# Performance work log

Measured on AMD Instinct MI355X. Metric: run time of the kernel, lower is better.

## Reference

```python
import jax, jax.numpy as jnp
import numpy as np

N_NODES = 100000
N_EDGES = 1600000
N_FEAT = 64
HIDDEN = 16


def setup_inputs() -> dict:
    key = jax.random.key(0)
    ks = jax.random.split(key, 10)
    x = jax.random.normal(ks[0], (N_NODES, N_FEAT), dtype=jnp.float32)
    edge_index = jax.random.randint(ks[1], (2, N_EDGES), 0, N_NODES, dtype=jnp.int64)
    As = jax.random.normal(ks[2], (2, N_EDGES), dtype=jnp.float32)
    ws_weights = jax.random.normal(ks[3], (2,), dtype=jnp.float32)
    Wl1 = jax.random.normal(ks[4], (N_FEAT, HIDDEN), dtype=jnp.float32) / np.sqrt(N_FEAT)
    bl1 = jnp.zeros((HIDDEN,), dtype=jnp.float32)
    Wr1 = jax.random.normal(ks[5], (N_FEAT, HIDDEN), dtype=jnp.float32) / np.sqrt(N_FEAT)
    Wl2 = jax.random.normal(ks[6], (HIDDEN, 1), dtype=jnp.float32) / np.sqrt(HIDDEN)
    bl2 = jnp.zeros((1,), dtype=jnp.float32)
    Wr2 = jax.random.normal(ks[7], (HIDDEN, 1), dtype=jnp.float32) / np.sqrt(HIDDEN)
    return {"x": x, "edge_index": edge_index, "As": As, "ws_weights": ws_weights,
            "Wl1": Wl1, "bl1": bl1, "Wr1": Wr1, "Wl2": Wl2, "bl2": bl2, "Wr2": Wr2}


def reference(x, edge_index, As, ws_weights, Wl1, bl1, Wr1, Wl2, bl2, Wr2):
    # WeightedSumLayer: weighted sum of per-edge weight vectors
    ewm = jnp.einsum('m,me->e', ws_weights, As)  # [E]
    # edge mask (nonzero weighted sum keeps the edge); instead of slicing to a
    # data-dependent edge count, zero out masked messages (same aggregation).
    mask = (ewm != 0).astype(x.dtype)  # [E]
    src, dst = edge_index[0], edge_index[1]
    n = x.shape[0]

    # SAGEConv layer 1 (aggr='sum'): out = lin_l(sum_j x_j) + lin_r(x)
    msg1 = x[src] * mask[:, None]                             # [E, F]
    agg1 = jax.ops.segment_sum(msg1, dst, num_segments=n)     # [N, F]
    h = jax.nn.relu(agg1 @ Wl1 + bl1 + x @ Wr1)               # [N, H]

    # SAGEConv layer 2
    msg2 = h[src] * mask[:, None]                             # [E, H]
    agg2 = jax.ops.segment_sum(msg2, dst, num_segments=n)     # [N, H]
    out = agg2 @ Wl2 + bl2 + h @ Wr2                          # [N, 1]
    return out
```

## Files before the change

### kernel.cpp

```cpp
#include <hip/hip_runtime.h>
#include <hip/hip_bf16.h>

constexpr int NN = 100000;
constexpr int NE = 1600000;
constexpr int NF = 64;
constexpr int NH = 16;

constexpr int NPB  = 128;
constexpr int LB   = 7;
constexpr int NBKT = (NN + NPB - 1) / NPB;
constexpr int CAP  = 2560;
constexpr int CHUNK = 8192;
constexpr int TB_B  = 512;
constexpr int NBLK_B = (NE + CHUNK - 1) / CHUNK;

__device__ __forceinline__ float bf16_to_f32(unsigned short u) {
    return __uint_as_float(((unsigned int)u) << 16);
}
__device__ __forceinline__ unsigned short f32_to_bf16(float f) {
    __hip_bfloat16 hb = __float2bfloat16(f);
    return *reinterpret_cast<unsigned short*>(&hb);
}

__global__ __launch_bounds__(256)
void k1_node_lin(const float* __restrict__ x,
                 const float* __restrict__ Wl1,
                 const float* __restrict__ Wr1,
                 unsigned short* __restrict__ p,
                 float* __restrict__ r)
{
    __shared__ float sW[2 * NF * NH];
    for (int i = threadIdx.x; i < NF * NH; i += 256) {
        sW[i]           = Wl1[i];
        sW[NF * NH + i] = Wr1[i];
    }
    __syncthreads();

    int n = blockIdx.x * 256 + threadIdx.x;
    if (n >= NN) return;

    float aL[NH], aR[NH];
#pragma unroll
    for (int j = 0; j < NH; ++j) { aL[j] = 0.f; aR[j] = 0.f; }

    const float4* xr = reinterpret_cast<const float4*>(x + (size_t)n * NF);
#pragma unroll
    for (int k4 = 0; k4 < NF / 4; ++k4) {
        float4 v = xr[k4];
        float xs[4] = {v.x, v.y, v.z, v.w};
#pragma unroll
        for (int t = 0; t < 4; ++t) {
            const float* wl = &sW[(k4 * 4 + t) * NH];
            const float* wr = &sW[NF * NH + (k4 * 4 + t) * NH];
#pragma unroll
            for (int j = 0; j < NH; ++j) {
                aL[j] = fmaf(xs[t], wl[j], aL[j]);
                aR[j] = fmaf(xs[t], wr[j], aR[j]);
            }
        }
    }

    unsigned int pu[8];
#pragma unroll
    for (int j2 = 0; j2 < 8; ++j2)
        pu[j2] = (unsigned int)f32_to_bf16(aL[2*j2]) |
                 ((unsigned int)f32_to_bf16(aL[2*j2+1]) << 16);
    uint4* pp = reinterpret_cast<uint4*>(p + (size_t)n * NH);
    pp[0] = make_uint4(pu[0], pu[1], pu[2], pu[3]);
    pp[1] = make_uint4(pu[4], pu[5], pu[6], pu[7]);

    float4* rp = reinterpret_cast<float4*>(r + (size_t)n * NH);
#pragma unroll
    for (int j4 = 0; j4 < NH / 4; ++j4)
        rp[j4] = make_float4(aR[j4*4], aR[j4*4+1], aR[j4*4+2], aR[j4*4+3]);
}

__global__ __launch_bounds__(TB_B)
void k_bucket(const int* __restrict__ ei, const float* __restrict__ As,
              const float* __restrict__ ws,
              int* __restrict__ bcnt, unsigned int* __restrict__ bmem)
{
    __shared__ unsigned int sw[CHUNK];
    __shared__ unsigned int srk[CHUNK];
    __shared__ int lcnt[NBKT];
    __shared__ int lbase[NBKT];
    int tid = threadIdx.x;
    for (int i = tid; i < NBKT; i += TB_B) lcnt[i] = 0;
    __syncthreads();

    int base = blockIdx.x * CHUNK;
    float w0 = ws[0], w1 = ws[1];

#pragma unroll
    for (int j = 0; j < CHUNK / TB_B; ++j) {
        int idx = j * TB_B + tid;
        int e = base + idx;
        unsigned int w = 0, rk = 0xFFFFFFFFu;
        if (e < NE) {
            float ewm = w0 * As[e] + w1 * As[NE + e];
            if (ewm != 0.f) {
                int dst = ei[NE + e];
                int bk  = dst >> LB;
                w  = ((unsigned)ei[e] << LB) | (unsigned)(dst & (NPB - 1));
                int rank = atomicAdd(&lcnt[bk], 1);
                rk = ((unsigned)bk << 13) | (unsigned)rank;
            }
        }
        sw[idx]  = w;
        srk[idx] = rk;
    }
    __syncthreads();

    for (int i = tid; i < NBKT; i += TB_B) {
        int c = lcnt[i];
        lbase[i] = c ? atomicAdd(&bcnt[i], c) : 0;
    }
    __syncthreads();

#pragma unroll
    for (int j = 0; j < CHUNK / TB_B; ++j) {
        int idx = j * TB_B + tid;
        unsigned int rk = srk[idx];
        if (rk != 0xFFFFFFFFu) {
            int bk   = rk >> 13;
            int rank = rk & 0x1FFF;
            int slot = lbase[bk] + rank;
            if (slot < CAP)
                bmem[(size_t)bk * CAP + slot] = sw[idx];
        }
    }
}

__global__ __launch_bounds__(256)
void k_agg1(const int* __restrict__ bcnt, unsigned int* __restrict__ bmem,
            const unsigned short* __restrict__ p, const float* __restrict__ r,
            const float* __restrict__ bl1, const float* __restrict__ Wl2,
            const float* __restrict__ bl2, const float* __restrict__ Wr2,
            float* __restrict__ q, float* __restrict__ out,
            int* __restrict__ gsoff)
{
    __shared__ unsigned int sbm[CAP];
    __shared__ unsigned int ssorted[CAP];
    __shared__ int hist[NPB];
    __shared__ int scan[NPB];
    __shared__ int soff[NPB + 1];

    int b = blockIdx.x;
    int tid = threadIdx.x;
    if (tid < NPB) hist[tid] = 0;
    __syncthreads();

    int cnt = min(bcnt[b], CAP);

    int rk[CAP / 256];
#pragma unroll
    for (int j = 0; j < CAP / 256; ++j) {
        int i = j * 256 + tid;
        if (i < cnt) {
            unsigned int w = bmem[(size_t)b * CAP + i];
            sbm[i] = w;
            rk[j] = atomicAdd(&hist[w & (NPB - 1)], 1);
        }
    }
    __syncthreads();

    if (tid < NPB) scan[tid] = hist[tid];
    __syncthreads();
    for (int off = 1; off < NPB; off <<= 1) {
        int u = (tid < NPB && tid >= off) ? scan[tid - off] : 0;
        __syncthreads();
        if (tid < NPB) scan[tid] += u;
        __syncthreads();
    }
    if (tid < NPB) soff[tid + 1] = scan[tid];
    if (tid == 0) soff[0] = 0;
    __syncthreads();

#pragma unroll
    for (int j = 0; j < CAP / 256; ++j) {
        int i = j * 256 + tid;
        if (i < cnt) {
            unsigned int w = sbm[i];
            ssorted[soff[w & (NPB - 1)] + rk[j]] = w;
        }
    }
    __syncthreads();

    for (int i = tid; i < cnt; i += 256)
        bmem[(size_t)b * CAP + i] = ssorted[i];
    if (tid < NPB + 1)
        gsoff[(size_t)b * (NPB + 1) + tid] = soff[tid];

    int g = tid >> 4, k = tid & 15;
    int n0 = b * NPB;
#pragma unroll
    for (int jj = 0; jj < 8; ++jj) {
        int nl = g * 8 + jj;
        int s = soff[nl], e = soff[nl + 1];
        float a = 0.f;
        int i = s;
        for (; i + 3 < e; i += 4) {
            unsigned w0 = ssorted[i], w1 = ssorted[i+1], w2 = ssorted[i+2], w3 = ssorted[i+3];
            float v0 = bf16_to_f32(p[(size_t)(w0 >> LB) * NH + k]);
            float v1 = bf16_to_f32(p[(size_t)(w1 >> LB) * NH + k]);
            float v2 = bf16_to_f32(p[(size_t)(w2 >> LB) * NH + k]);
            float v3 = bf16_to_f32(p[(size_t)(w3 >> LB) * NH + k]);
            a += (v0 + v1) + (v2 + v3);
        }
        for (; i < e; ++i)
            a += bf16_to_f32(p[(size_t)(ssorted[i] >> LB) * NH + k]);

        int n = n0 + nl;
        if (n < NN) {
            float h = a + r[(size_t)n * NH + k] + bl1[k];
            h = h > 0.f ? h : 0.f;
            float qv = h * Wl2[k];
            float sv = h * Wr2[k];
#pragma unroll
            for (int m = 8; m >= 1; m >>= 1) {
                qv += __shfl_xor(qv, m);
                sv += __shfl_xor(sv, m);
            }
            if (k == 0) {
                q[n]   = qv;
                out[n] = sv + bl2[0];
            }
        }
    }
}

__global__ __launch_bounds__(256)
void k_agg2(const int* __restrict__ gsoff, const unsigned int* __restrict__ bmem,
            const float* __restrict__ q, float* __restrict__ out)
{
    int n = blockIdx.x * 256 + threadIdx.x;
    if (n >= NN) return;
    int b  = n >> LB;
    int dl = n & (NPB - 1);
    int s = gsoff[(size_t)b * (NPB + 1) + dl];
    int e = gsoff[(size_t)b * (NPB + 1) + dl + 1];
    const unsigned int* bm = bmem + (size_t)b * CAP;

    float a = 0.f;
    int i = s;
    for (; i + 3 < e; i += 4) {
        unsigned w0 = bm[i], w1 = bm[i+1], w2 = bm[i+2], w3 = bm[i+3];
        a += (q[w0 >> LB] + q[w1 >> LB]) + (q[w2 >> LB] + q[w3 >> LB]);
    }
    for (; i < e; ++i)
        a += q[bm[i] >> LB];
    out[n] += a;
}

extern "C" void kernel_launch(void* const* d_in, const int* in_sizes, int n_in,
                              void* d_out, int out_size, void* d_ws, size_t ws_size,
                              hipStream_t stream)
{
    const float* x   = (const float*)d_in[0];
    const int*   ei  = (const int*)  d_in[1];
    const float* As  = (const float*)d_in[2];
    const float* ws  = (const float*)d_in[3];
    const float* Wl1 = (const float*)d_in[4];
    const float* bl1 = (const float*)d_in[5];
    const float* Wr1 = (const float*)d_in[6];
    const float* Wl2 = (const float*)d_in[7];
    const float* bl2 = (const float*)d_in[8];
    const float* Wr2 = (const float*)d_in[9];
    float* out = (float*)d_out;

    unsigned short* p     = (unsigned short*)d_ws;
    float*          r     = (float*)(p + (size_t)NN * NH);
    float*          q     = r + (size_t)NN * NH;
    int*            bcnt  = (int*)(q + NN);
    int*            gsoff = bcnt + NBKT;
    unsigned int*   bmem  = (unsigned int*)(gsoff + (size_t)NBKT * (NPB + 1));

    hipMemsetAsync(bcnt, 0, NBKT * sizeof(int), stream);

    k1_node_lin<<<(NN + 255) / 256, 256, 0, stream>>>(x, Wl1, Wr1, p, r);
    k_bucket<<<NBLK_B, TB_B, 0, stream>>>(ei, As, ws, bcnt, bmem);
    k_agg1<<<NBKT, 256, 0, stream>>>(bcnt, bmem, p, r, bl1, Wl2, bl2, Wr2, q, out, gsoff);
    k_agg2<<<(NN + 255) / 256, 256, 0, stream>>>(gsoff, bmem, q, out);
}
```

Baseline: 181.0 us.

## Fuse node-linear and edge-bucketing kernels into one interleaved-role launch

```diff
diff --git a/kernel.cpp b/kernel.cpp
--- a/kernel.cpp
+++ b/kernel.cpp
@@ -10,9 +10,12 @@
 constexpr int LB   = 7;
 constexpr int NBKT = (NN + NPB - 1) / NPB;
 constexpr int CAP  = 2560;
-constexpr int CHUNK = 8192;
-constexpr int TB_B  = 512;
-constexpr int NBLK_B = (NE + CHUNK - 1) / CHUNK;
+constexpr int CHUNK = 4096;
+constexpr int NBLK_B  = (NE + CHUNK - 1) / CHUNK;
+constexpr int NBLK_K1 = (NN + 255) / 256;
+
+constexpr int SMEM_BYTES = (CHUNK * 2 + 2 * NBKT * 4) > (2 * NF * NH * 4)
+                         ? (CHUNK * 2 + 2 * NBKT * 4) : (2 * NF * NH * 4);
 
 __device__ __forceinline__ float bf16_to_f32(unsigned short u) {
     return __uint_as_float(((unsigned int)u) << 16);
@@ -23,110 +26,109 @@
 }
 
 __global__ __launch_bounds__(256)
-void k1_node_lin(const float* __restrict__ x,
-                 const float* __restrict__ Wl1,
-                 const float* __restrict__ Wr1,
-                 unsigned short* __restrict__ p,
-                 float* __restrict__ r)
-{
-    __shared__ float sW[2 * NF * NH];
-    for (int i = threadIdx.x; i < NF * NH; i += 256) {
-        sW[i]           = Wl1[i];
-        sW[NF * NH + i] = Wr1[i];
-    }
-    __syncthreads();
-
-    int n = blockIdx.x * 256 + threadIdx.x;
-    if (n >= NN) return;
-
-    float aL[NH], aR[NH];
-#pragma unroll
-    for (int j = 0; j < NH; ++j) { aL[j] = 0.f; aR[j] = 0.f; }
-
-    const float4* xr = reinterpret_cast<const float4*>(x + (size_t)n * NF);
-#pragma unroll
-    for (int k4 = 0; k4 < NF / 4; ++k4) {
-        float4 v = xr[k4];
-        float xs[4] = {v.x, v.y, v.z, v.w};
-#pragma unroll
-        for (int t = 0; t < 4; ++t) {
-            const float* wl = &sW[(k4 * 4 + t) * NH];
-            const float* wr = &sW[NF * NH + (k4 * 4 + t) * NH];
-#pragma unroll
-            for (int j = 0; j < NH; ++j) {
-                aL[j] = fmaf(xs[t], wl[j], aL[j]);
-                aR[j] = fmaf(xs[t], wr[j], aR[j]);
-            }
-        }
-    }
-
-    unsigned int pu[8];
-#pragma unroll
-    for (int j2 = 0; j2 < 8; ++j2)
-        pu[j2] = (unsigned int)f32_to_bf16(aL[2*j2]) |
-                 ((unsigned int)f32_to_bf16(aL[2*j2+1]) << 16);
-    uint4* pp = reinterpret_cast<uint4*>(p + (size_t)n * NH);
-    pp[0] = make_uint4(pu[0], pu[1], pu[2], pu[3]);
-    pp[1] = make_uint4(pu[4], pu[5], pu[6], pu[7]);
-
-    float4* rp = reinterpret_cast<float4*>(r + (size_t)n * NH);
-#pragma unroll
-    for (int j4 = 0; j4 < NH / 4; ++j4)
-        rp[j4] = make_float4(aR[j4*4], aR[j4*4+1], aR[j4*4+2], aR[j4*4+3]);
-}
-
-__global__ __launch_bounds__(TB_B)
-void k_bucket(const int* __restrict__ ei, const float* __restrict__ As,
-              const float* __restrict__ ws,
-              int* __restrict__ bcnt, unsigned int* __restrict__ bmem)
-{
-    __shared__ unsigned int sw[CHUNK];
-    __shared__ unsigned int srk[CHUNK];
-    __shared__ int lcnt[NBKT];
-    __shared__ int lbase[NBKT];
-    int tid = threadIdx.x;
-    for (int i = tid; i < NBKT; i += TB_B) lcnt[i] = 0;
-    __syncthreads();
-
-    int base = blockIdx.x * CHUNK;
-    float w0 = ws[0], w1 = ws[1];
-
-#pragma unroll
-    for (int j = 0; j < CHUNK / TB_B; ++j) {
-        int idx = j * TB_B + tid;
-        int e = base + idx;
-        unsigned int w = 0, rk = 0xFFFFFFFFu;
-        if (e < NE) {
-            float ewm = w0 * As[e] + w1 * As[NE + e];
-            if (ewm != 0.f) {
+void k_fused(const float* __restrict__ x,
+             const float* __restrict__ Wl1,
+             const float* __restrict__ Wr1,
+             unsigned short* __restrict__ p,
+             float* __restrict__ r,
+             const int* __restrict__ ei, const float* __restrict__ As,
+             const float* __restrict__ ws,
+             int* __restrict__ bcnt, unsigned int* __restrict__ bmem)
+{
+    __shared__ __align__(16) char smem[SMEM_BYTES];
+    int role = blockIdx.x & 1;
+    int rb   = blockIdx.x >> 1;
+    int tid  = threadIdx.x;
+
+    if (role == 0) {
+        float* sW = (float*)smem;
+        for (int i = tid; i < NF * NH; i += 256) {
+            sW[i]           = Wl1[i];
+            sW[NF * NH + i] = Wr1[i];
+        }
+        __syncthreads();
+
+        int n = rb * 256 + tid;
+        if (n >= NN) return;
+
+        float aL[NH], aR[NH];
+#pragma unroll
+        for (int j = 0; j < NH; ++j) { aL[j] = 0.f; aR[j] = 0.f; }
+
+        const float4* xr = reinterpret_cast<const float4*>(x + (size_t)n * NF);
+#pragma unroll
+        for (int k4 = 0; k4 < NF / 4; ++k4) {
+            float4 v = xr[k4];
+            float xs[4] = {v.x, v.y, v.z, v.w};
+#pragma unroll
+            for (int t = 0; t < 4; ++t) {
+                const float* wl = &sW[(k4 * 4 + t) * NH];
+                const float* wr = &sW[NF * NH + (k4 * 4 + t) * NH];
+#pragma unroll
+                for (int j = 0; j < NH; ++j) {
+                    aL[j] = fmaf(xs[t], wl[j], aL[j]);
+                    aR[j] = fmaf(xs[t], wr[j], aR[j]);
+                }
+            }
+        }
+
+        unsigned int pu[8];
+#pragma unroll
+        for (int j2 = 0; j2 < 8; ++j2)
+            pu[j2] = (unsigned int)f32_to_bf16(aL[2*j2]) |
+                     ((unsigned int)f32_to_bf16(aL[2*j2+1]) << 16);
+        uint4* pp = reinterpret_cast<uint4*>(p + (size_t)n * NH);
+        pp[0] = make_uint4(pu[0], pu[1], pu[2], pu[3]);
+        pp[1] = make_uint4(pu[4], pu[5], pu[6], pu[7]);
+
+        float4* rp = reinterpret_cast<float4*>(r + (size_t)n * NH);
+#pragma unroll
+        for (int j4 = 0; j4 < NH / 4; ++j4)
+            rp[j4] = make_float4(aR[j4*4], aR[j4*4+1], aR[j4*4+2], aR[j4*4+3]);
+    } else {
+        unsigned short* srk = (unsigned short*)smem;
+        int* lcnt  = (int*)(smem + CHUNK * 2);
+        int* lbase = lcnt + NBKT;
+
+        for (int i = tid; i < NBKT; i += 256) lcnt[i] = 0;
+        __syncthreads();
+
+        int base = rb * CHUNK;
+        float w0 = ws[0], w1 = ws[1];
+
+#pragma unroll
+        for (int j = 0; j < CHUNK / 256; ++j) {
+            int idx = j * 256 + tid;
+            int e = base + idx;
+            unsigned short rk = 0xFFFFu;
+            if (e < NE) {
+                float ewm = w0 * As[e] + w1 * As[NE + e];
+                if (ewm != 0.f)
+                    rk = (unsigned short)atomicAdd(&lcnt[ei[NE + e] >> LB], 1);
+            }
+            srk[idx] = rk;
+        }
+        __syncthreads();
+
+        for (int i = tid; i < NBKT; i += 256) {
+            int c = lcnt[i];
+            lbase[i] = c ? atomicAdd(&bcnt[i], c) : 0;
+        }
+        __syncthreads();
+
+#pragma unroll
+        for (int j = 0; j < CHUNK / 256; ++j) {
+            int idx = j * 256 + tid;
+            unsigned short rk = srk[idx];
+            if (rk != 0xFFFFu) {
+                int e   = base + idx;
                 int dst = ei[NE + e];
                 int bk  = dst >> LB;
-                w  = ((unsigned)ei[e] << LB) | (unsigned)(dst & (NPB - 1));
-                int rank = atomicAdd(&lcnt[bk], 1);
-                rk = ((unsigned)bk << 13) | (unsigned)rank;
-            }
-        }
-        sw[idx]  = w;
-        srk[idx] = rk;
-    }
-    __syncthreads();
-
-    for (int i = tid; i < NBKT; i += TB_B) {
-        int c = lcnt[i];
-        lbase[i] = c ? atomicAdd(&bcnt[i], c) : 0;
-    }
-    __syncthreads();
-
-#pragma unroll
-    for (int j = 0; j < CHUNK / TB_B; ++j) {
-        int idx = j * TB_B + tid;
-        unsigned int rk = srk[idx];
-        if (rk != 0xFFFFFFFFu) {
-            int bk   = rk >> 13;
-            int rank = rk & 0x1FFF;
-            int slot = lbase[bk] + rank;
-            if (slot < CAP)
-                bmem[(size_t)bk * CAP + slot] = sw[idx];
+                int slot = lbase[bk] + rk;
+                if (slot < CAP)
+                    bmem[(size_t)bk * CAP + slot] =
+                        ((unsigned)ei[e] << LB) | (unsigned)(dst & (NPB - 1));
+            }
         }
     }
 }
@@ -277,8 +279,8 @@
 
     hipMemsetAsync(bcnt, 0, NBKT * sizeof(int), stream);
 
-    k1_node_lin<<<(NN + 255) / 256, 256, 0, stream>>>(x, Wl1, Wr1, p, r);
-    k_bucket<<<NBLK_B, TB_B, 0, stream>>>(ei, As, ws, bcnt, bmem);
+    int nblk = 2 * ((NBLK_B > NBLK_K1) ? NBLK_B : NBLK_K1);
+    k_fused<<<nblk, 256, 0, stream>>>(x, Wl1, Wr1, p, r, ei, As, ws, bcnt, bmem);
     k_agg1<<<NBKT, 256, 0, stream>>>(bcnt, bmem, p, r, bl1, Wl2, bl2, Wr2, q, out, gsoff);
     k_agg2<<<(NN + 255) / 256, 256, 0, stream>>>(gsoff, bmem, q, out);
 }
```

Result: no change. 178.7 us (-1.3%).
